# Kernel tuning notes

Hardware: AMD Instinct MI355X
Metric: run time of the kernel (lower is better)

Reference implementation:

```python
import jax, jax.numpy as jnp
import numpy as np

M, N, B, L = 512, 2048, 4, 20
H_DENSITY = 0.02  # Tanner graph sparsity: row weight ~N*p=40, col weight ~M*p=10


def setup_inputs() -> dict:
    key = jax.random.key(0)
    ks = jax.random.split(key, 10)
    H = jax.random.bernoulli(ks[0], H_DENSITY, (M, N)).astype(jnp.float32)
    llrs = jax.random.uniform(ks[1], (N,), jnp.float32)
    syndromes = jax.random.randint(ks[2], (B, M, 1), 0, 2, jnp.int32)
    errors = jax.random.randint(ks[3], (B, N), 0, 2, jnp.int32)
    weights_de = jax.random.uniform(ks[4], (L, M, N), jnp.float32)
    weights_llr = jax.random.uniform(ks[5], (L, N), jnp.float32)
    marg_weights_de = jax.random.uniform(ks[6], (L, M, N), jnp.float32)
    marg_weights_llr = jax.random.uniform(ks[7], (L, N), jnp.float32)
    rhos = jnp.ones((L,), jnp.float32)
    residual_weights = jnp.zeros((L,), jnp.float32)
    return dict(syndromes=syndromes, errors=errors, H=H, llrs=llrs,
                weights_de=weights_de, weights_llr=weights_llr,
                marg_weights_de=marg_weights_de, marg_weights_llr=marg_weights_llr,
                rhos=rhos, residual_weights=residual_weights)


def reference(syndromes, errors, H, llrs, weights_de, weights_llr,
              marg_weights_de, marg_weights_llr, rhos, residual_weights):
    batch = syndromes.shape[0]
    m, n = H.shape
    rhos_norm = jax.nn.softmax(rhos)                       # (L,)
    sign = 1.0 - 2.0 * syndromes.astype(H.dtype)           # (B,m,1): (-1)**syndrome
    err_f = errors.astype(H.dtype)                         # (B,n)
    eps = 1e-6

    def step(msgs_dn, xs):
        w_de, w_llr, mw_de, mw_llr, rho, rw = xs
        # error-node (variable) update: column-sum minus self, masked by H
        msgs_en = (H * (llrs * w_llr)
                   + jnp.sum(msgs_dn * w_de, axis=1, keepdims=True)) * H - msgs_dn
        # detector-node (check) update: tanh-product rule with self-exclusion
        d = jnp.tanh(msgs_en * 0.5)
        d = jnp.where(d == 0, jnp.asarray(1.0, d.dtype), d)
        d = jnp.clip(d, -1.0 + eps, 1.0 - eps)
        row_prod = jnp.prod(d, axis=2, keepdims=True)      # (B,m,1)
        msgs_new = 2.0 * jnp.arctanh(row_prod / d) * (sign * H) + rw * msgs_dn
        # marginal beliefs and weighted BCE loss
        beliefs = jnp.sum(msgs_new * mw_de, axis=1) + llrs * mw_llr   # (B,n)
        loss_b = jnp.sum(jax.nn.softplus(beliefs) - (1.0 - err_f) * beliefs, axis=1)
        return msgs_new, rho * loss_b

    init = jnp.zeros((batch, m, n), H.dtype)
    _, losses = jax.lax.scan(
        step, init,
        (weights_de, weights_llr, marg_weights_de, marg_weights_llr,
         rhos_norm, residual_weights))
    return jnp.sum(losses) / batch
```

## Files before the change

### kernel.cpp

```cpp
#include <hip/hip_runtime.h>

#define MM 512
#define NN 2048
#define BB 4
#define LL 20
#define MAXDEG 128
#define NT    1024
#define RR    16
#define NBLK  64
#define COLSB 128
#define SLOTS 2048
#define EPT   2
#define EPSV  1e-6f

#define WS_ROW_DEG   0
#define WS_ROW_PAD   2048
#define WS_ROW_OFFF  264192
#define WS_RPTR_RB   266240
#define WS_EDGE_CS   299072
#define WS_PP        430144
#define WS_BAR       692288

__device__ __forceinline__ void pre_barrier(int* ctr) {
    __syncthreads();
    if (threadIdx.x == 0) {
        __threadfence();
        __hip_atomic_fetch_add(ctr, 1, __ATOMIC_RELAXED, __HIP_MEMORY_SCOPE_AGENT);
        int it = 0;
        while (__hip_atomic_load(ctr, __ATOMIC_RELAXED, __HIP_MEMORY_SCOPE_AGENT) < NBLK) {
            __builtin_amdgcn_s_sleep(1);
            if (++it > (1 << 22)) break;
        }
        __threadfence();
    }
    __syncthreads();
}

__device__ __forceinline__ void grid_barrier(int* ctr) {
    __syncthreads();
    if (threadIdx.x == 0) {
        asm volatile("s_waitcnt vmcnt(0)" ::: "memory");
        __hip_atomic_fetch_add(ctr, 1, __ATOMIC_RELAXED, __HIP_MEMORY_SCOPE_AGENT);
        int it = 0;
        while (__hip_atomic_load(ctr, __ATOMIC_RELAXED, __HIP_MEMORY_SCOPE_AGENT) < RR) {
            __builtin_amdgcn_s_sleep(1);
            if (++it > (1 << 22)) break;
        }
        asm volatile("" ::: "memory");
    }
    __syncthreads();
}

__global__ __launch_bounds__(NT)
void nbp_all(const int* __restrict__ synd, const int* __restrict__ errs,
             const float* __restrict__ H, const float* __restrict__ llrs,
             const float* __restrict__ w_de, const float* __restrict__ w_llr,
             const float* __restrict__ mw_de, const float* __restrict__ mw_llr,
             const float* __restrict__ rhos, const float* __restrict__ resw,
             int* __restrict__ row_deg, int* __restrict__ row_pad,
             float* __restrict__ row_offf, int* __restrict__ rptr_rb,
             unsigned* __restrict__ edge_cs,
             float* __restrict__ pp, int* __restrict__ bar,
             float* __restrict__ out) {
    __shared__ float d_sb[SLOTS];
    __shared__ int   tmp_s[MM];
    __shared__ float colsum_s[COLSB];
    __shared__ float bel_s[COLSB];
    __shared__ float ncs_s[COLSB];
    __shared__ float llrs_s[COLSB];
    __shared__ float ef_s[COLSB];
    __shared__ float rowprod_s[MM];
    __shared__ float rp_coef[MM];
    __shared__ int   rowptr_s[MM + 1];
    __shared__ float rho_n[LL];
    __shared__ float red[16];

    const int blk = blockIdx.x;
    const int b = blk & 3, r = blk >> 2;
    const int tid = threadIdx.x;
    const int lane = tid & 63, wave = tid >> 6;
    int* bar_b = bar + b * 64;
    int* pbar  = bar + BB * 64;

    if (blk == 0 && tid == 0)
        __hip_atomic_store(out, 0.0f, __ATOMIC_RELAXED, __HIP_MEMORY_SCOPE_AGENT);

    if (wave < 8) {
        int i = blk * 8 + wave;
        const float* hrow = H + (size_t)i * NN;
        int base = 0;
        for (int pass = 0; pass < 4; ++pass) {
            float v[8];
            #pragma unroll
            for (int c = 0; c < 8; ++c) v[c] = hrow[(pass * 8 + c) * 64 + lane];
            #pragma unroll
            for (int c = 0; c < 8; ++c) {
                bool pred = v[c] != 0.0f;
                unsigned long long mask = __ballot(pred);
                int before = __popcll(mask & ((1ull << lane) - 1ull));
                if (pred) {
                    int k = base + before;
                    if (k < MAXDEG) row_pad[i * MAXDEG + k] = (pass * 8 + c) * 64 + lane;
                }
                base += __popcll(mask);
            }
        }
        if (lane == 0) {
            row_deg[i] = base < MAXDEG ? base : MAXDEG;
            row_offf[i] = powf(1.0f - EPSV, (float)(NN - base));
        }
    }
    pre_barrier(&pbar[0]);

    if (blk < RR) {
        const int slice = blk;
        if (tid < MM) {
            int deg = row_deg[tid], cnt = 0;
            for (int k = 0; k < deg; ++k)
                cnt += ((row_pad[tid * MAXDEG + k] >> 7) == slice);
            tmp_s[tid] = cnt;
        }
        __syncthreads();
        for (int off = 1; off < MM; off <<= 1) {
            int v = (tid < MM && tid >= off) ? tmp_s[tid - off] : 0;
            __syncthreads();
            if (tid < MM) tmp_s[tid] += v;
            __syncthreads();
        }
        if (tid == 0) rptr_rb[slice * 513] = 0;
        if (tid < MM) rptr_rb[slice * 513 + tid + 1] = tmp_s[tid];
        __syncthreads();
        if (tid < MM) {
            int deg = row_deg[tid];
            int pos = (tid == 0) ? 0 : tmp_s[tid - 1];
            for (int k = 0; k < deg; ++k) {
                int c = row_pad[tid * MAXDEG + k];
                if ((c >> 7) == slice && pos < SLOTS) {
                    edge_cs[slice * SLOTS + pos] = ((unsigned)tid << 16) | (unsigned)c;
                    ++pos;
                }
            }
        }
    }
    pre_barrier(&pbar[1]);

    if (tid == 0) {
        float mx = -1e30f;
        for (int l = 0; l < LL; ++l) mx = fmaxf(mx, rhos[l]);
        float s = 0.0f;
        for (int l = 0; l < LL; ++l) { float e = __expf(rhos[l] - mx); rho_n[l] = e; s += e; }
        for (int l = 0; l < LL; ++l) rho_n[l] /= s;
    }
    if (tid < MM) {
        rowptr_s[tid] = rptr_rb[r * 513 + tid];
        rp_coef[tid] = row_offf[tid] * (1.0f - 2.0f * (float)synd[b * MM + tid]);
    }
    if (tid == MM) rowptr_s[MM] = rptr_rb[r * 513 + MM];
    if (tid < COLSB) {
        int j = r * COLSB + tid;
        float lj = llrs[j];
        llrs_s[tid] = lj;
        colsum_s[tid] = lj * w_llr[j];
        ef_s[tid] = 1.0f - (float)errs[b * NN + j];
        bel_s[tid] = 0.0f;
        ncs_s[tid] = 0.0f;
    }

    int cnt = rptr_rb[r * 513 + MM];
    if (cnt > SLOTS) cnt = SLOTS;
    const int s0 = EPT * tid;

    unsigned idx[EPT];
    float msg[EPT], d_r[EPT];
    #pragma unroll
    for (int k = 0; k < EPT; ++k) {
        int e = r * SLOTS + s0 + k;
        idx[k] = edge_cs[(s0 + k) < cnt ? e : r * SLOTS];
        msg[k] = 0.0f;
    }
    __syncthreads();

    float loss = 0.0f;

    for (int l = 0; l < LL; ++l) {
        const float rw = resw[l];
        const int par = l & 1;
        float* pp_b = pp + ((size_t)par * BB + b) * RR * MM;

        float mv[EPT], wn[EPT];
        {
            const float* mwl = mw_de + (size_t)l * (MM * NN);
            const float* wl  = w_de + (size_t)(l + 1) * (MM * NN);
            #pragma unroll
            for (int k = 0; k < EPT; ++k) {
                size_t eo = (size_t)(idx[k] >> 16) * NN + (idx[k] & 0xffffu);
                mv[k] = mwl[eo];
                wn[k] = (l + 1 < LL) ? wl[eo] : 0.0f;
            }
        }

        #pragma unroll
        for (int k = 0; k < EPT; ++k) {
            int jl = idx[k] & (COLSB - 1);
            float en = colsum_s[jl] - msg[k];
            float t = __expf(en);
            float d = 1.0f - 2.0f * __builtin_amdgcn_rcpf(t + 1.0f);
            if (d == 0.0f) d = 1.0f;
            d = fminf(fmaxf(d, -1.0f + EPSV), 1.0f - EPSV);
            d_r[k] = d;
        }
        *(float2*)&d_sb[s0] = make_float2(d_r[0], d_r[1]);
        __syncthreads();

        if (tid < MM) {
            int lo = rowptr_s[tid], hi = rowptr_s[tid + 1];
            if (hi > SLOTS) hi = SLOTS;
            float p = 1.0f;
            for (int s = lo; s < hi; ++s) p *= d_sb[s];
            __hip_atomic_store(&pp_b[r * MM + tid], p,
                               __ATOMIC_RELAXED, __HIP_MEMORY_SCOPE_AGENT);
        }
        grid_barrier(&bar_b[l]);

        if (tid < MM) {
            float p = rp_coef[tid];
            #pragma unroll
            for (int r2 = 0; r2 < RR; ++r2)
                p *= __hip_atomic_load(&pp_b[r2 * MM + tid],
                                       __ATOMIC_RELAXED, __HIP_MEMORY_SCOPE_AGENT);
            rowprod_s[tid] = p;
        }
        __syncthreads();

        #pragma unroll
        for (int k = 0; k < EPT; ++k) {
            int il = idx[k] >> 16;
            int jl = idx[k] & (COLSB - 1);
            float rq = rowprod_s[il] * __builtin_amdgcn_rcpf(d_r[k]);
            float v = __logf(1.0f + rq) - __logf(1.0f - rq) + rw * msg[k];
            msg[k] = v;
            if (s0 + k < cnt) {
                atomicAdd(&bel_s[jl], v * mv[k]);
                if (l + 1 < LL) atomicAdd(&ncs_s[jl], v * wn[k]);
            }
        }
        __syncthreads();

        if (tid < COLSB) {
            int j = r * COLSB + tid;
            float bel = llrs_s[tid] * mw_llr[l * NN + j] + bel_s[tid];
            bel_s[tid] = 0.0f;
            float sp = fmaxf(bel, 0.0f) + log1pf(__expf(-fabsf(bel)));
            loss += rho_n[l] * (sp - ef_s[tid] * bel);
            if (l + 1 < LL) {
                colsum_s[tid] = llrs_s[tid] * w_llr[(l + 1) * NN + j] + ncs_s[tid];
                ncs_s[tid] = 0.0f;
            }
        }
        __syncthreads();
    }

    #pragma unroll
    for (int off = 32; off > 0; off >>= 1) loss += __shfl_down(loss, off);
    if (lane == 0) red[wave] = loss;
    __syncthreads();
    if (wave == 0) {
        float v = (lane < 16) ? red[lane] : 0.0f;
        #pragma unroll
        for (int off = 8; off > 0; off >>= 1) v += __shfl_down(v, off);
        if (lane == 0) atomicAdd(out, v * 0.25f);
    }
}

extern "C" void kernel_launch(void* const* d_in, const int* in_sizes, int n_in,
                              void* d_out, int out_size, void* d_ws, size_t ws_size,
                              hipStream_t stream) {
    const int*   synd  = (const int*)  d_in[0];
    const int*   errs  = (const int*)  d_in[1];
    const float* H     = (const float*)d_in[2];
    const float* llrs  = (const float*)d_in[3];
    const float* w_de  = (const float*)d_in[4];
    const float* w_llr = (const float*)d_in[5];
    const float* mw_de = (const float*)d_in[6];
    const float* mw_llr= (const float*)d_in[7];
    const float* rhos  = (const float*)d_in[8];
    const float* resw  = (const float*)d_in[9];

    char* ws = (char*)d_ws;
    int*      row_deg  = (int*)     (ws + WS_ROW_DEG);
    int*      row_pad  = (int*)     (ws + WS_ROW_PAD);
    float*    row_offf = (float*)   (ws + WS_ROW_OFFF);
    int*      rptr_rb  = (int*)     (ws + WS_RPTR_RB);
    unsigned* edge_cs  = (unsigned*)(ws + WS_EDGE_CS);
    float*    pp       = (float*)   (ws + WS_PP);
    int*      bar      = (int*)     (ws + WS_BAR);
    float*    out      = (float*)d_out;

    hipMemsetAsync(bar, 0, (BB * 64 + 64) * sizeof(int), stream);

    nbp_all<<<NBLK, NT, 0, stream>>>(synd, errs, H, llrs, w_de, w_llr, mw_de, mw_llr,
                                     rhos, resw, row_deg, row_pad, row_offf, rptr_rb,
                                     edge_cs, pp, bar, out);
}
```

Before: 439.5 us.

## Prepack per-edge weights into compact workspace and split row-product reduction

Adds a prologue phase in which all blocks gather the sparse w_de and mw_de values for every layer and slice into contiguous per-slot arrays. The main loop then loads them as coalesced float2 reads instead of scattered loads into the large dense weight tensors. It also splits the cross-block partial-product reduction over two threads per row and combines them with a shuffle. The cost is an extra grid barrier plus a one-time scattered gather pass and about 5 MB of extra workspace. Note that the gather is still scattered, only moved out of the per-layer critical path.

```diff
diff --git a/kernel.cpp b/kernel.cpp
--- a/kernel.cpp
+++ b/kernel.cpp
@@ -18,8 +18,10 @@
 #define WS_ROW_OFFF  264192
 #define WS_RPTR_RB   266240
 #define WS_EDGE_CS   299072
-#define WS_PP        430144
-#define WS_BAR       692288
+#define WS_WDE_P     430144
+#define WS_MWDE_P    3051584
+#define WS_PP        5673024
+#define WS_BAR       5935168
 
 __device__ __forceinline__ void pre_barrier(int* ctr) {
     __syncthreads();
@@ -60,6 +62,7 @@
              int* __restrict__ row_deg, int* __restrict__ row_pad,
              float* __restrict__ row_offf, int* __restrict__ rptr_rb,
              unsigned* __restrict__ edge_cs,
+             float* __restrict__ wde_p, float* __restrict__ mwde_p,
              float* __restrict__ pp, int* __restrict__ bar,
              float* __restrict__ out) {
     __shared__ float d_sb[SLOTS];
@@ -144,6 +147,27 @@
     }
     pre_barrier(&pbar[1]);
 
+    for (int pr = blk; pr < LL * RR; pr += NBLK) {
+        int l = pr / RR, slc = pr - l * RR;
+        int tot = rptr_rb[slc * 513 + MM];
+        if (tot > SLOTS) tot = SLOTS;
+        const float* wl  = w_de + (size_t)l * (MM * NN);
+        const float* mwl = mw_de + (size_t)l * (MM * NN);
+        for (int s = tid; s < SLOTS; s += NT) {
+            size_t di = (size_t)pr * SLOTS + s;
+            if (s < tot) {
+                unsigned pk = edge_cs[slc * SLOTS + s];
+                size_t eo = (size_t)(pk >> 16) * NN + (pk & 0xffffu);
+                wde_p[di]  = wl[eo];
+                mwde_p[di] = mwl[eo];
+            } else {
+                wde_p[di]  = 0.0f;
+                mwde_p[di] = 0.0f;
+            }
+        }
+    }
+    pre_barrier(&pbar[2]);
+
     if (tid == 0) {
         float mx = -1e30f;
         for (int l = 0; l < LL; ++l) mx = fmaxf(mx, rhos[l]);
@@ -187,17 +211,12 @@
         const int par = l & 1;
         float* pp_b = pp + ((size_t)par * BB + b) * RR * MM;
 
-        float mv[EPT], wn[EPT];
-        {
-            const float* mwl = mw_de + (size_t)l * (MM * NN);
-            const float* wl  = w_de + (size_t)(l + 1) * (MM * NN);
-            #pragma unroll
-            for (int k = 0; k < EPT; ++k) {
-                size_t eo = (size_t)(idx[k] >> 16) * NN + (idx[k] & 0xffffu);
-                mv[k] = mwl[eo];
-                wn[k] = (l + 1 < LL) ? wl[eo] : 0.0f;
-            }
-        }
+        const float2 mq = *(const float2*)(mwde_p + ((size_t)(l * RR + r) * SLOTS) + s0);
+        float2 wq = make_float2(0.f, 0.f);
+        if (l + 1 < LL)
+            wq = *(const float2*)(wde_p + ((size_t)((l + 1) * RR + r) * SLOTS) + s0);
+        const float mv[2] = {mq.x, mq.y};
+        const float wn[2] = {wq.x, wq.y};
 
         #pragma unroll
         for (int k = 0; k < EPT; ++k) {
@@ -222,13 +241,17 @@
         }
         grid_barrier(&bar_b[l]);
 
-        if (tid < MM) {
-            float p = rp_coef[tid];
+        {
+            int row = tid >> 1, half = tid & 1;
+            float p = 1.0f;
             #pragma unroll
-            for (int r2 = 0; r2 < RR; ++r2)
-                p *= __hip_atomic_load(&pp_b[r2 * MM + tid],
+            for (int q = 0; q < RR / 2; ++q) {
+                int r2 = q * 2 + half;
+                p *= __hip_atomic_load(&pp_b[r2 * MM + row],
                                        __ATOMIC_RELAXED, __HIP_MEMORY_SCOPE_AGENT);
-            rowprod_s[tid] = p;
+            }
+            p *= __shfl_xor(p, 1);
+            if (half == 0) rowprod_s[row] = p * rp_coef[row];
         }
         __syncthreads();
 
@@ -292,6 +315,8 @@
     float*    row_offf = (float*)   (ws + WS_ROW_OFFF);
     int*      rptr_rb  = (int*)     (ws + WS_RPTR_RB);
     unsigned* edge_cs  = (unsigned*)(ws + WS_EDGE_CS);
+    float*    wde_p    = (float*)   (ws + WS_WDE_P);
+    float*    mwde_p   = (float*)   (ws + WS_MWDE_P);
     float*    pp       = (float*)   (ws + WS_PP);
     int*      bar      = (int*)     (ws + WS_BAR);
     float*    out      = (float*)d_out;
@@ -300,5 +325,5 @@
 
     nbp_all<<<NBLK, NT, 0, stream>>>(synd, errs, H, llrs, w_de, w_llr, mw_de, mw_llr,
                                      rhos, resw, row_deg, row_pad, row_offf, rptr_rb,
-                                     edge_cs, pp, bar, out);
+                                     edge_cs, wde_p, mwde_p, pp, bar, out);
 }
```

Result: faster. 395.3 us (-10.0%).
